# Optimization experiments

Hardware: AMD Instinct MI355X
Metric: run time of the kernel (lower is better)

## Reference

```python
import jax, jax.numpy as jnp
import numpy as np

FEATURES_M = 1_000_000
HIDDEN = 64
LAYERS = [128, 64]
BATCH = 16384
N_FIELDS = 50


def setup_inputs() -> dict:
    key = jax.random.key(0)
    ks = jax.random.split(key, 12)
    inp = {
        "features": jax.random.randint(ks[0], (BATCH, N_FIELDS), 0, FEATURES_M, dtype=jnp.int32),
        "labels": jax.random.normal(ks[1], (BATCH, 1), dtype=jnp.float32),
        # learned parameters
        "emb_table": jax.random.normal(ks[2], (FEATURES_M, HIDDEN), dtype=jnp.float32) * 0.01,
        "bias_table": jax.random.normal(ks[3], (FEATURES_M, 1), dtype=jnp.float32) * 0.01,
        "w_bias": jax.random.normal(ks[4], (1, 1), dtype=jnp.float32),  # Dense(1, use_bias=False)
        "W1": jax.random.normal(ks[5], (HIDDEN, LAYERS[0]), dtype=jnp.float32) * (1.0 / np.sqrt(HIDDEN)),
        "b1": jnp.zeros((LAYERS[0],), dtype=jnp.float32),
        "W2": jax.random.normal(ks[6], (LAYERS[0], LAYERS[1]), dtype=jnp.float32) * (1.0 / np.sqrt(LAYERS[0])),
        "b2": jnp.zeros((LAYERS[1],), dtype=jnp.float32),
        "Wp": jax.random.normal(ks[7], (LAYERS[1], 1), dtype=jnp.float32) * (1.0 / np.sqrt(LAYERS[1])),
        "bp": jnp.zeros((1,), dtype=jnp.float32),
    }
    return inp


def reference(features, labels, emb_table, bias_table, w_bias, W1, b1, W2, b2, Wp, bp):
    # Embedding gather: [B, F, D]
    nonzero_emb = emb_table[features]
    # FM bi-interaction pooling: 0.5 * ((sum e)^2 - sum(e^2))  -> [B, D]
    summed = jnp.sum(nonzero_emb, axis=1)
    squared_sum = jnp.sum(jnp.square(nonzero_emb), axis=1)
    fm = 0.5 * (jnp.square(summed) - squared_sum)
    # Deep MLP stack (batch_norm off, dropout identity at eval keep_prob=1)
    h = jax.nn.relu(fm @ W1 + b1)
    h = jax.nn.relu(h @ W2 + b2)
    pred = h @ Wp + bp  # [B, 1]
    bilinear = jnp.sum(pred, axis=1, keepdims=True)  # [B, 1]
    # First-order feature bias: gather [B, F, 1] then sum over fields
    feature_bias = jnp.sum(bias_table[features], axis=1)  # [B, 1]
    # Global bias: Dense(1, no bias) applied to ones_like(labels)
    global_bias = jnp.ones_like(labels) @ w_bias  # [B, 1]
    return bilinear + feature_bias + global_bias
```

## Files before the change

kernel.cpp:

```cpp
#include <hip/hip_runtime.h>


#define NFIELDS 50
#define HIDDEN  64
#define L1N     128
#define L2N     64
#define RPW     4
#define WAVES   4
#define ROWS_PER_BLOCK (RPW * WAVES)

__global__ __launch_bounds__(256, 4) void neuralfm_kernel(
    const int*   __restrict__ features,
    const float* __restrict__ emb,
    const float* __restrict__ bias_t,
    const float* __restrict__ w_bias,
    const float* __restrict__ W1,
    const float* __restrict__ b1,
    const float* __restrict__ W2,
    const float* __restrict__ b2,
    const float* __restrict__ Wp,
    const float* __restrict__ bp,
    float*       __restrict__ out)
{
    __shared__ int    sIdx[WAVES][RPW * NFIELDS];
    __shared__ float4 sFm4[WAVES][RPW * HIDDEN / 4];
    __shared__ float  sH1 [WAVES][RPW * L1N];

    const int tid  = threadIdx.x;
    const int wave = tid >> 6;
    const int lane = tid & 63;
    const int sub  = lane >> 4;
    const int le   = lane & 15;
    const int row0 = blockIdx.x * ROWS_PER_BLOCK + wave * RPW;

    const int idx_base = row0 * NFIELDS;
    #pragma unroll
    for (int t = lane; t < RPW * NFIELDS; t += 64)
        sIdx[wave][t] = features[idx_base + t];
    __syncthreads();

    float biasacc[RPW];
    #pragma unroll
    for (int r = 0; r < RPW; ++r) biasacc[r] = 0.f;
    if (lane < NFIELDS) {
        #pragma unroll
        for (int r = 0; r < RPW; ++r)
            biasacc[r] = bias_t[sIdx[wave][r * NFIELDS + lane]];
    }

    const float4* __restrict__ emb4 = (const float4*)emb;
    float sx = 0.f, sy = 0.f, sz = 0.f, sw = 0.f;
    float qx = 0.f, qy = 0.f, qz = 0.f, qw = 0.f;
    const int* myIdx = &sIdx[wave][sub * NFIELDS];
    #pragma unroll
    for (int f = 0; f < NFIELDS; ++f) {
        const int    idx = myIdx[f];
        const float4 v   = emb4[(size_t)idx * (HIDDEN / 4) + le];
        sx += v.x; sy += v.y; sz += v.z; sw += v.w;
        qx += v.x * v.x; qy += v.y * v.y; qz += v.z * v.z; qw += v.w * v.w;
    }
    float4 fm;
    fm.x = 0.5f * (sx * sx - qx);
    fm.y = 0.5f * (sy * sy - qy);
    fm.z = 0.5f * (sz * sz - qz);
    fm.w = 0.5f * (sw * sw - qw);
    sFm4[wave][sub * (HIDDEN / 4) + le] = fm;
    __syncthreads();

    float h1a[RPW], h1b[RPW];
    #pragma unroll
    for (int r = 0; r < RPW; ++r) { h1a[r] = 0.f; h1b[r] = 0.f; }

    for (int dq = 0; dq < HIDDEN / 4; ++dq) {
        float w0[4], w1[4];
        #pragma unroll
        for (int c = 0; c < 4; ++c) {
            w0[c] = W1[(4 * dq + c) * L1N + lane];
            w1[c] = W1[(4 * dq + c) * L1N + 64 + lane];
        }
        #pragma unroll
        for (int r = 0; r < RPW; ++r) {
            const float4 fv = sFm4[wave][r * (HIDDEN / 4) + dq];
            h1a[r] += fv.x * w0[0] + fv.y * w0[1] + fv.z * w0[2] + fv.w * w0[3];
            h1b[r] += fv.x * w1[0] + fv.y * w1[1] + fv.z * w1[2] + fv.w * w1[3];
        }
    }
    const float bias1a = b1[lane];
    const float bias1b = b1[64 + lane];
    #pragma unroll
    for (int r = 0; r < RPW; ++r) {
        sH1[wave][r * L1N + lane]      = fmaxf(h1a[r] + bias1a, 0.f);
        sH1[wave][r * L1N + 64 + lane] = fmaxf(h1b[r] + bias1b, 0.f);
    }
    __syncthreads();

    const float4* sH14 = (const float4*)&sH1[wave][0];
    float h2[RPW];
    #pragma unroll
    for (int r = 0; r < RPW; ++r) h2[r] = 0.f;

    for (int jq = 0; jq < L1N / 4; ++jq) {
        float w[4];
        #pragma unroll
        for (int c = 0; c < 4; ++c)
            w[c] = W2[(4 * jq + c) * L2N + lane];
        #pragma unroll
        for (int r = 0; r < RPW; ++r) {
            const float4 hv = sH14[r * (L1N / 4) + jq];
            h2[r] += hv.x * w[0] + hv.y * w[1] + hv.z * w[2] + hv.w * w[3];
        }
    }
    const float bias2 = b2[lane];
    const float wp    = Wp[lane];

    float tot[RPW];
    #pragma unroll
    for (int r = 0; r < RPW; ++r)
        tot[r] = fmaxf(h2[r] + bias2, 0.f) * wp + biasacc[r];

    #pragma unroll
    for (int r = 0; r < RPW; ++r) {
        float v = tot[r];
        #pragma unroll
        for (int off = 32; off > 0; off >>= 1)
            v += __shfl_xor(v, off, 64);
        tot[r] = v;
    }
    if (lane == 0) {
        const float c = bp[0] + w_bias[0];
        #pragma unroll
        for (int r = 0; r < RPW; ++r)
            out[row0 + r] = tot[r] + c;
    }
}

extern "C" void kernel_launch(void* const* d_in, const int* in_sizes, int n_in,
                              void* d_out, int out_size, void* d_ws, size_t ws_size,
                              hipStream_t stream) {
    const int*   features = (const int*)  d_in[0];
    const float* emb      = (const float*)d_in[2];
    const float* bias_t   = (const float*)d_in[3];
    const float* w_bias   = (const float*)d_in[4];
    const float* W1       = (const float*)d_in[5];
    const float* b1       = (const float*)d_in[6];
    const float* W2       = (const float*)d_in[7];
    const float* b2       = (const float*)d_in[8];
    const float* Wp       = (const float*)d_in[9];
    const float* bp       = (const float*)d_in[10];
    float*       out      = (float*)d_out;

    const int batch  = in_sizes[0] / NFIELDS;
    const int blocks = batch / ROWS_PER_BLOCK;

    neuralfm_kernel<<<blocks, 256, 0, stream>>>(
        features, emb, bias_t, w_bias, W1, b1, W2, b2, Wp, bp, out);
}
```

Baseline: 354.5 us.

## Halve rows per wave, split field gather across half-waves, drop block barriers

Each wave now handles 2 batch rows instead of 4. The two 32-lane halves of the wave each gather alternating fields, which halves the serial length of the embedding gather loop. The partial sums and squares are combined with a cross-half shuffle before the FM term is written to shared memory. The block-wide __syncthreads calls are removed, because each wave only touches its own shared-memory slice. The trade-off is twice as many blocks, with W1/W2 reloaded per wave for fewer rows, and the code now depends on intra-wave ordering of LDS accesses for correctness.

```diff
diff --git a/kernel.cpp b/kernel.cpp
--- a/kernel.cpp
+++ b/kernel.cpp
@@ -5,7 +5,7 @@
 #define HIDDEN  64
 #define L1N     128
 #define L2N     64
-#define RPW     4
+#define RPW     2
 #define WAVES   4
 #define ROWS_PER_BLOCK (RPW * WAVES)
 
@@ -29,47 +29,53 @@
     const int tid  = threadIdx.x;
     const int wave = tid >> 6;
     const int lane = tid & 63;
-    const int sub  = lane >> 4;
     const int le   = lane & 15;
+    const int r    = (lane >> 4) & 1;
+    const int fg   = lane >> 5;
     const int row0 = blockIdx.x * ROWS_PER_BLOCK + wave * RPW;
 
     const int idx_base = row0 * NFIELDS;
     #pragma unroll
     for (int t = lane; t < RPW * NFIELDS; t += 64)
         sIdx[wave][t] = features[idx_base + t];
-    __syncthreads();
 
     float biasacc[RPW];
     #pragma unroll
-    for (int r = 0; r < RPW; ++r) biasacc[r] = 0.f;
+    for (int r2 = 0; r2 < RPW; ++r2) biasacc[r2] = 0.f;
     if (lane < NFIELDS) {
         #pragma unroll
-        for (int r = 0; r < RPW; ++r)
-            biasacc[r] = bias_t[sIdx[wave][r * NFIELDS + lane]];
+        for (int r2 = 0; r2 < RPW; ++r2)
+            biasacc[r2] = bias_t[sIdx[wave][r2 * NFIELDS + lane]];
     }
 
     const float4* __restrict__ emb4 = (const float4*)emb;
+    const int* myIdx = &sIdx[wave][r * NFIELDS];
     float sx = 0.f, sy = 0.f, sz = 0.f, sw = 0.f;
     float qx = 0.f, qy = 0.f, qz = 0.f, qw = 0.f;
-    const int* myIdx = &sIdx[wave][sub * NFIELDS];
     #pragma unroll
-    for (int f = 0; f < NFIELDS; ++f) {
-        const int    idx = myIdx[f];
+    for (int i = 0; i < NFIELDS / 2; ++i) {
+        const int    idx = myIdx[2 * i + fg];
         const float4 v   = emb4[(size_t)idx * (HIDDEN / 4) + le];
         sx += v.x; sy += v.y; sz += v.z; sw += v.w;
         qx += v.x * v.x; qy += v.y * v.y; qz += v.z * v.z; qw += v.w * v.w;
     }
-    float4 fm;
-    fm.x = 0.5f * (sx * sx - qx);
-    fm.y = 0.5f * (sy * sy - qy);
-    fm.z = 0.5f * (sz * sz - qz);
-    fm.w = 0.5f * (sw * sw - qw);
-    sFm4[wave][sub * (HIDDEN / 4) + le] = fm;
-    __syncthreads();
+    sx += __shfl_xor(sx, 32, 64); sy += __shfl_xor(sy, 32, 64);
+    sz += __shfl_xor(sz, 32, 64); sw += __shfl_xor(sw, 32, 64);
+    qx += __shfl_xor(qx, 32, 64); qy += __shfl_xor(qy, 32, 64);
+    qz += __shfl_xor(qz, 32, 64); qw += __shfl_xor(qw, 32, 64);
+
+    if (fg == 0) {
+        float4 fm;
+        fm.x = 0.5f * (sx * sx - qx);
+        fm.y = 0.5f * (sy * sy - qy);
+        fm.z = 0.5f * (sz * sz - qz);
+        fm.w = 0.5f * (sw * sw - qw);
+        sFm4[wave][r * (HIDDEN / 4) + le] = fm;
+    }
 
     float h1a[RPW], h1b[RPW];
     #pragma unroll
-    for (int r = 0; r < RPW; ++r) { h1a[r] = 0.f; h1b[r] = 0.f; }
+    for (int r2 = 0; r2 < RPW; ++r2) { h1a[r2] = 0.f; h1b[r2] = 0.f; }
 
     for (int dq = 0; dq < HIDDEN / 4; ++dq) {
         float w0[4], w1[4];
@@ -79,25 +85,24 @@
             w1[c] = W1[(4 * dq + c) * L1N + 64 + lane];
         }
         #pragma unroll
-        for (int r = 0; r < RPW; ++r) {
-            const float4 fv = sFm4[wave][r * (HIDDEN / 4) + dq];
-            h1a[r] += fv.x * w0[0] + fv.y * w0[1] + fv.z * w0[2] + fv.w * w0[3];
-            h1b[r] += fv.x * w1[0] + fv.y * w1[1] + fv.z * w1[2] + fv.w * w1[3];
+        for (int r2 = 0; r2 < RPW; ++r2) {
+            const float4 fv = sFm4[wave][r2 * (HIDDEN / 4) + dq];
+            h1a[r2] += fv.x * w0[0] + fv.y * w0[1] + fv.z * w0[2] + fv.w * w0[3];
+            h1b[r2] += fv.x * w1[0] + fv.y * w1[1] + fv.z * w1[2] + fv.w * w1[3];
         }
     }
     const float bias1a = b1[lane];
     const float bias1b = b1[64 + lane];
     #pragma unroll
-    for (int r = 0; r < RPW; ++r) {
-        sH1[wave][r * L1N + lane]      = fmaxf(h1a[r] + bias1a, 0.f);
-        sH1[wave][r * L1N + 64 + lane] = fmaxf(h1b[r] + bias1b, 0.f);
+    for (int r2 = 0; r2 < RPW; ++r2) {
+        sH1[wave][r2 * L1N + lane]      = fmaxf(h1a[r2] + bias1a, 0.f);
+        sH1[wave][r2 * L1N + 64 + lane] = fmaxf(h1b[r2] + bias1b, 0.f);
     }
-    __syncthreads();
 
     const float4* sH14 = (const float4*)&sH1[wave][0];
     float h2[RPW];
     #pragma unroll
-    for (int r = 0; r < RPW; ++r) h2[r] = 0.f;
+    for (int r2 = 0; r2 < RPW; ++r2) h2[r2] = 0.f;
 
     for (int jq = 0; jq < L1N / 4; ++jq) {
         float w[4];
@@ -105,9 +110,9 @@
         for (int c = 0; c < 4; ++c)
             w[c] = W2[(4 * jq + c) * L2N + lane];
         #pragma unroll
-        for (int r = 0; r < RPW; ++r) {
-            const float4 hv = sH14[r * (L1N / 4) + jq];
-            h2[r] += hv.x * w[0] + hv.y * w[1] + hv.z * w[2] + hv.w * w[3];
+        for (int r2 = 0; r2 < RPW; ++r2) {
+            const float4 hv = sH14[r2 * (L1N / 4) + jq];
+            h2[r2] += hv.x * w[0] + hv.y * w[1] + hv.z * w[2] + hv.w * w[3];
         }
     }
     const float bias2 = b2[lane];
@@ -115,22 +120,22 @@
 
     float tot[RPW];
     #pragma unroll
-    for (int r = 0; r < RPW; ++r)
-        tot[r] = fmaxf(h2[r] + bias2, 0.f) * wp + biasacc[r];
+    for (int r2 = 0; r2 < RPW; ++r2)
+        tot[r2] = fmaxf(h2[r2] + bias2, 0.f) * wp + biasacc[r2];
 
     #pragma unroll
-    for (int r = 0; r < RPW; ++r) {
-        float v = tot[r];
+    for (int r2 = 0; r2 < RPW; ++r2) {
+        float v = tot[r2];
         #pragma unroll
         for (int off = 32; off > 0; off >>= 1)
             v += __shfl_xor(v, off, 64);
-        tot[r] = v;
+        tot[r2] = v;
     }
     if (lane == 0) {
         const float c = bp[0] + w_bias[0];
         #pragma unroll
-        for (int r = 0; r < RPW; ++r)
-            out[row0 + r] = tot[r] + c;
+        for (int r2 = 0; r2 < RPW; ++r2)
+            out[row0 + r2] = tot[r2] + c;
     }
 }
 
```

After: 356.3 us. About the same (+0.5%).
